# Optimization experiments

Hardware: AMD Instinct MI355X
Metric: run time of the kernel (lower is better)

The kernel has to match this reference:

```python
import jax, jax.numpy as jnp
import numpy as np

B, N = 1, 512
NODE_DIM, EDGE_DIM = 384, 128
H, SK, SV, PK, PV = 8, 16, 16, 4, 4
EPS = 1e-8
LN_EPS = 1e-5


def setup_inputs() -> dict:
    key = jax.random.key(0)
    ks = jax.random.split(key, 20)
    d, e = NODE_DIM, EDGE_DIM
    s = 0.02
    rn = lambda k, sh: jax.random.normal(k, sh, jnp.float32) * s
    # orthonormal per-residue rotations (valid rigid frames)
    R, _ = jnp.linalg.qr(jax.random.normal(ks[2], (B, N, 3, 3), jnp.float32))
    out_dim = H * (SV + EDGE_DIM + PV * 4)  # scalar + pairwise + points(3) + point norms(1)
    return dict(
        node_features=jax.random.normal(ks[0], (B, N, d), jnp.float32),
        edge_features=jax.random.normal(ks[1], (B, N, N, e), jnp.float32),
        rotations=R,
        translations=jax.random.normal(ks[3], (B, N, 3), jnp.float32),
        mask=jnp.ones((B, N), bool),
        Wq_s=rn(ks[4], (d, H * SK)), Wk_s=rn(ks[5], (d, H * SK)), Wv_s=rn(ks[6], (d, H * SV)),
        Wq_p=rn(ks[7], (d, H * PK * 3)), Wk_p=rn(ks[8], (d, H * PK * 3)), Wv_p=rn(ks[9], (d, H * PV * 3)),
        point_weights=jnp.full((H,), np.log(np.e - 1.0), jnp.float32),  # softplus -> 1
        Wb=rn(ks[10], (e, H)), bb=jnp.zeros((H,), jnp.float32),
        Wo=rn(ks[11], (out_dim, d)), bo=jnp.zeros((d,), jnp.float32),
        g1=jnp.ones((d,), jnp.float32), beta1=jnp.zeros((d,), jnp.float32),
        W1=rn(ks[12], (d, 2 * d)), b1=jnp.zeros((2 * d,), jnp.float32),
        W2=rn(ks[13], (2 * d, 2 * d)), b2=jnp.zeros((2 * d,), jnp.float32),
        W3=rn(ks[14], (2 * d, d)), b3=jnp.zeros((d,), jnp.float32),
        g2=jnp.ones((d,), jnp.float32), beta2=jnp.zeros((d,), jnp.float32),
    )


def _layer_norm(x, g, b):
    mu = x.mean(-1, keepdims=True)
    var = ((x - mu) ** 2).mean(-1, keepdims=True)
    return (x - mu) * jax.lax.rsqrt(var + LN_EPS) * g + b


def _forward(node_features, edge_features, rotations, translations, mask,
             Wq_s, Wk_s, Wv_s, Wq_p, Wk_p, Wv_p, point_weights, Wb, bb, Wo, bo,
             g1, beta1, W1, b1, W2, b2, W3, b3, g2, beta2):
    b, n, d = node_features.shape
    # num_attn_logits = 3 (scalar + point + pairwise)
    scal_scale = (3 * SK) ** -0.5
    point_scale = (3 * PK * 4.5) ** -0.5
    pair_scale = 3 ** -0.5

    qs = (node_features @ Wq_s).reshape(b, n, H, SK)
    kk = (node_features @ Wk_s).reshape(b, n, H, SK)
    vs = (node_features @ Wv_s).reshape(b, n, H, SV)

    def apply_rigid(p):  # p: (b,n,h,d,3); global = R^T applied per lucidrains einsum + t
        return jnp.einsum('bnhdc,bncr->bnhdr', p, rotations) + translations[:, :, None, None, :]

    qp = apply_rigid((node_features @ Wq_p).reshape(b, n, H, PK, 3))
    kp = apply_rigid((node_features @ Wk_p).reshape(b, n, H, PK, 3))
    vp = apply_rigid((node_features @ Wv_p).reshape(b, n, H, PV, 3))

    logits = jnp.einsum('bihk,bjhk->bhij', qs, kk) * scal_scale

    # point distance term: sum_{d,c} (q-k)^2 = |q|^2 + |k|^2 - 2 q.k (avoids (b,h,i,j,d,3) tensor)
    w = jax.nn.softplus(point_weights)  # (H,)
    q2 = jnp.einsum('bnhdc,bnhdc->bhn', qp, qp)
    k2 = jnp.einsum('bnhdc,bnhdc->bhn', kp, kp)
    cross = jnp.einsum('bihdc,bjhdc->bhij', qp, kp)
    dist = q2[..., :, None] + k2[..., None, :] - 2.0 * cross  # (b,h,i,j)
    logits = logits - 0.5 * point_scale * w[None, :, None, None] * dist

    pair_bias = (jnp.einsum('bije,eh->bhij', edge_features, Wb) + bb[None, :, None, None]) * pair_scale
    logits = logits + pair_bias

    pm = mask[:, None, :, None] & mask[:, None, None, :]  # (b,1,i,j)
    logits = jnp.where(pm, logits, -jnp.finfo(logits.dtype).max)
    attn = jax.nn.softmax(logits, axis=-1)  # (b,h,i,j)

    rs = jnp.einsum('bhij,bjhv->bihv', attn, vs).reshape(b, n, H * SV)
    rp = jnp.einsum('bhij,bije->bihe', attn, edge_features).reshape(b, n, H * EDGE_DIM)
    pts = jnp.einsum('bhij,bjhdc->bihdc', attn, vp)
    # invert rigid: subtract t, apply R (inverse of R^T application)
    local = jnp.einsum('bihdc,birc->bihdr', pts - translations[:, :, None, None, :], rotations)
    norms = jnp.sqrt((local ** 2).sum(-1) + EPS)  # (b,n,H,PV)

    cat = jnp.concatenate([rs, local.reshape(b, n, H * PV * 3), norms.reshape(b, n, H * PV), rp], axis=-1)
    ipa_out = cat @ Wo + bo

    x = _layer_norm(ipa_out, g1, beta1)  # dropout is identity at eval
    x = jax.nn.relu(x @ W1 + b1)
    x = jax.nn.relu(x @ W2 + b2)
    x = x @ W3 + b3
    return _layer_norm(x, g2, beta2)


def reference(node_features, edge_features, rotations, translations, mask,
              Wq_s, Wk_s, Wv_s, Wq_p, Wk_p, Wv_p, point_weights, Wb, bb, Wo, bo,
              g1, beta1, W1, b1, W2, b2, W3, b3, g2, beta2):
    return _forward(node_features, edge_features, rotations, translations, mask,
                    Wq_s, Wk_s, Wv_s, Wq_p, Wk_p, Wv_p, point_weights, Wb, bb, Wo, bo,
                    g1, beta1, W1, b1, W2, b2, W3, b3, g2, beta2)
```

## Files before the change

### kernel.cpp

```cpp
#include <hip/hip_runtime.h>
#include <cstddef>

#define NN 512
#define DD 384
#define EE 128
#define HH 8
#define JSPLIT 16

static constexpr float SCAL_SCALE  = 0.1443375673f;
static constexpr float POINT_SCALE = 0.1360827635f;
static constexpr float PAIR_SCALE  = 0.5773502692f;
static constexpr float LN_EPS = 1e-5f;
static constexpr float EPS    = 1e-8f;

typedef __bf16 bf16x8 __attribute__((ext_vector_type(8)));
typedef float  f32x4  __attribute__((ext_vector_type(4)));

__device__ __forceinline__ unsigned short bf16_bits(float v) {
    union { __bf16 b; unsigned short s; } c; c.b = (__bf16)v; return c.s;
}
__device__ __forceinline__ float bits2f(unsigned u) {
    union { unsigned u; float f; } c; c.u = u; return c.f;
}

__global__ __launch_bounds__(256) void prep_weights_kernel(
    const float* __restrict__ Wo, const float* __restrict__ W1,
    const float* __restrict__ W2, const float* __restrict__ W3,
    const float* __restrict__ Wq_s, const float* __restrict__ Wk_s,
    const float* __restrict__ Wv_s,
    const float* __restrict__ Wq_p, const float* __restrict__ Wk_p,
    const float* __restrict__ Wv_p, const float* __restrict__ nf,
    unsigned short* __restrict__ WoT, unsigned short* __restrict__ W1T,
    unsigned short* __restrict__ W2T, unsigned short* __restrict__ W3T,
    unsigned short* __restrict__ WprojT, unsigned short* __restrict__ nfb)
{
    const int b = blockIdx.x;
    if (b >= 1884) {
        const int idx = (b - 1884) * 1024 + threadIdx.x * 4;
        float4 v = *(const float4*)(nf + idx);
        unsigned lo = bf16_bits(v.x) | ((unsigned)bf16_bits(v.y) << 16);
        unsigned hi = bf16_bits(v.z) | ((unsigned)bf16_bits(v.w) << 16);
        uint2 pk; pk.x = lo; pk.y = hi;
        *(uint2*)(nfb + idx) = pk;
        return;
    }
    const float* W; unsigned short* out;
    int K, N, tile, rowoff = 0;
    if (b < 480)       { W = Wo;   out = WoT;    K = 1280; N = 384; tile = b; }
    else if (b < 768)  { W = W1;   out = W1T;    K = 384;  N = 768; tile = b - 480; }
    else if (b < 1344) { W = W2;   out = W2T;    K = 768;  N = 768; tile = b - 768; }
    else if (b < 1632) { W = W3;   out = W3T;    K = 768;  N = 384; tile = b - 1344; }
    else if (b < 1680) { W = Wq_s; out = WprojT; K = 384;  N = 128; tile = b - 1632; rowoff = 0; }
    else if (b < 1728) { W = Wk_s; out = WprojT; K = 384;  N = 128; tile = b - 1680; rowoff = 128; }
    else if (b < 1776) { W = Wv_s; out = WprojT; K = 384;  N = 128; tile = b - 1728; rowoff = 256; }
    else if (b < 1812) { W = Wq_p; out = WprojT; K = 384;  N = 96;  tile = b - 1776; rowoff = 384; }
    else if (b < 1848) { W = Wk_p; out = WprojT; K = 384;  N = 96;  tile = b - 1812; rowoff = 480; }
    else               { W = Wv_p; out = WprojT; K = 384;  N = 96;  tile = b - 1848; rowoff = 576; }

    const int ntn = N / 32;
    const int n0 = (tile % ntn) * 32, k0 = (tile / ntn) * 32;
    __shared__ float tb[32][33];
    const int tx = threadIdx.x & 31, ty = threadIdx.x >> 5;
    #pragma unroll
    for (int dy = 0; dy < 32; dy += 8)
        tb[ty + dy][tx] = W[(size_t)(k0 + ty + dy) * N + n0 + tx];
    __syncthreads();
    #pragma unroll
    for (int dy = 0; dy < 32; dy += 8)
        out[(size_t)(rowoff + n0 + ty + dy) * K + k0 + tx] = bf16_bits(tb[tx][ty + dy]);
}

template <int K, int NOUT, bool RELU, bool HASB, bool OUTBF>
__global__ __launch_bounds__(256) void gemm_bf16(
    const unsigned short* __restrict__ Xb, const unsigned short* __restrict__ Wt,
    const float* __restrict__ bias, void* __restrict__ Yv)
{
    const int t = threadIdx.x;
    const int w = t >> 6, lane = t & 63;
    const int r = lane & 15, q = lane >> 4;
    const int n0 = blockIdx.x * 16;
    const int m0 = blockIdx.y * 64 + w * 16;

    const unsigned short* xrow = Xb + (size_t)(m0 + r) * K + q * 8;
    const unsigned short* wrow = Wt + (size_t)(n0 + r) * K + q * 8;

    f32x4 acc = {0.f, 0.f, 0.f, 0.f};
    #pragma unroll 4
    for (int k0 = 0; k0 < K; k0 += 32) {
        union { uint4 u; bf16x8 v; } au, bu;
        au.u = *(const uint4*)(xrow + k0);
        bu.u = *(const uint4*)(wrow + k0);
        acc = __builtin_amdgcn_mfma_f32_16x16x32_bf16(au.v, bu.v, acc, 0, 0, 0);
    }
    const int n = n0 + r;
    const float bi = HASB ? bias[n] : 0.f;
    #pragma unroll
    for (int reg = 0; reg < 4; reg++) {
        const int m = m0 + q * 4 + reg;
        float v = acc[reg] + bi;
        if (RELU) v = fmaxf(v, 0.f);
        if (OUTBF) ((unsigned short*)Yv)[(size_t)m * NOUT + n] = bf16_bits(v);
        else       ((float*)Yv)[(size_t)m * NOUT + n] = v;
    }
}

__global__ __launch_bounds__(256) void ipa_post_kernel(
    const float* __restrict__ proj_out, const float* __restrict__ rot,
    const float* __restrict__ trans, const float* __restrict__ pw,
    const float* __restrict__ bb,
    unsigned short* __restrict__ Qp, unsigned short* __restrict__ Kp,
    unsigned short* __restrict__ svT)
{
    const int i = blockIdx.x;
    const int t = threadIdx.x;
    __shared__ float outs[672];
    __shared__ float ptg[288];
    __shared__ float q2s[8], k2s[8], pwh[8];

    for (int f = t; f < 672; f += 256) outs[f] = proj_out[(size_t)i * 672 + f];
    if (t < 8) pwh[t] = 0.5f * POINT_SCALE * log1pf(expf(pw[t]));
    __syncthreads();

    for (int f = t; f < 288; f += 256) {
        int which = f / 96, idx = f % 96;
        int hd = idx / 3, r = idx % 3;
        float acc = trans[(size_t)i * 3 + r];
        #pragma unroll
        for (int c = 0; c < 3; c++)
            acc += outs[384 + which * 96 + hd * 3 + c] * rot[(size_t)i * 9 + c * 3 + r];
        ptg[f] = acc;
    }
    __syncthreads();
    if (t < 16) {
        int which = t / 8, h = t % 8;
        float acc = 0.f;
        #pragma unroll
        for (int m = 0; m < 12; m++) {
            float v = ptg[which * 96 + h * 12 + m];
            acc += v * v;
        }
        (which ? k2s : q2s)[h] = acc;
    }
    __syncthreads();

    {
        const int h = t >> 5, d = t & 31;
        float qv, kv;
        if (d < 16)      { qv = outs[h * 16 + d] * SCAL_SCALE; kv = outs[128 + h * 16 + d]; }
        else if (d < 28) { qv = ptg[h * 12 + d - 16] * (2.f * pwh[h]); kv = ptg[96 + h * 12 + d - 16]; }
        else if (d == 28){ qv = -pwh[h] * q2s[h]; kv = 1.f; }
        else if (d == 29){ qv = 1.f; kv = -pwh[h] * k2s[h]; }
        else if (d == 30){ qv = 1.f; kv = bb[h] * PAIR_SCALE; }
        else             { qv = 0.f; kv = 0.f; }
        Qp[((size_t)i * 8 + h) * 32 + d] = bf16_bits(qv);
        Kp[((size_t)i * 8 + h) * 32 + d] = bf16_bits(kv);
    }
    if (t < 128) {
        int h = t >> 4, v = t & 15;
        svT[((size_t)h * 32 + v) * NN + i] = bf16_bits(outs[256 + h * 16 + v]);
    } else if (t < 224) {
        int idx = t - 128, h = idx / 12, m = idx % 12;
        svT[((size_t)h * 32 + 16 + m) * NN + i] = bf16_bits(ptg[192 + idx]);
    }
}

__global__ __launch_bounds__(256) void ipa_fused2(
    const float* __restrict__ edge,
    const unsigned short* __restrict__ Qp, const unsigned short* __restrict__ Kp,
    const unsigned short* __restrict__ svT, const float* __restrict__ Wb,
    float* __restrict__ Opart, float* __restrict__ Mpart, float* __restrict__ Lpart)
{
    const int js = blockIdx.x;
    const int it = blockIdx.y;
    const int i0 = it * 8;
    const int jbase = js * 32;
    const int t = threadIdx.x;
    const int w = t >> 6, lane = t & 63;
    const int r = lane & 15, q = lane >> 4;

    __shared__ unsigned short wbT[16 * 128];
    __shared__ unsigned short edA[64 * 128];
    __shared__ float Lqk[64 * 37];
    __shared__ float Lb[64 * 9];
    __shared__ unsigned short svj[8 * 8 * 32];
    __shared__ float mrow[64], lrow[64], arow[64];

    for (int idx = t; idx < 2048; idx += 256) {
        int h = idx >> 7, e = idx & 127;
        wbT[idx] = bf16_bits((h < 8) ? Wb[e * 8 + h] * PAIR_SCALE : 0.f);
    }
    if (t < 64) { mrow[t] = -1e30f; lrow[t] = 0.f; }
    __syncthreads();

    bf16x8 wbf[4];
    #pragma unroll
    for (int s = 0; s < 4; s++)
        wbf[s] = *(const bf16x8*)&wbT[r * 128 + s * 32 + q * 8];

    #pragma unroll
    for (int hh = 0; hh < 2; hh++) {
        const int h = w * 2 + hh;
        bf16x8 aq = *(const bf16x8*)&Qp[((size_t)(i0 + (r & 7)) * 8 + h) * 32 + q * 8];
        #pragma unroll
        for (int jt = 0; jt < 2; jt++) {
            bf16x8 bk = *(const bf16x8*)&Kp[((size_t)(jbase + jt * 16 + r) * 8 + h) * 32 + q * 8];
            f32x4 acc = {0.f, 0.f, 0.f, 0.f};
            acc = __builtin_amdgcn_mfma_f32_16x16x32_bf16(aq, bk, acc, 0, 0, 0);
            if (q < 2) {
                #pragma unroll
                for (int reg = 0; reg < 4; reg++)
                    Lqk[(h * 8 + q * 4 + reg) * 37 + jt * 16 + r] = acc[reg];
            }
        }
    }

    const int sj = t >> 5, sih = (t >> 4) & 1, sseg = t & 15;
    const int hsv = t / 28, csv = t % 28;
    float4 pf[8];
    uint4 svpf;
    {
        const int j0 = jbase;
        #pragma unroll
        for (int il = 0; il < 4; il++) {
            const float* src = edge + (((size_t)(i0 + sih * 4 + il) * NN) + (j0 + sj)) * EE + sseg * 8;
            pf[il * 2]     = *(const float4*)src;
            pf[il * 2 + 1] = *(const float4*)(src + 4);
        }
        if (t < 224) svpf = *(const uint4*)&svT[(size_t)(hsv * 32 + csv) * NN + j0];
    }

    const int ai = t >> 5, ah = (t >> 2) & 7, ap = t & 3;
    const int prow = ah * 8 + ai;
    float rp[32];
    float sva[8];
    #pragma unroll
    for (int z = 0; z < 32; z++) rp[z] = 0.f;
    #pragma unroll
    for (int s = 0; s < 8; s++) sva[s] = 0.f;

    for (int st = 0; st < 4; st++) {
        __syncthreads();
        #pragma unroll
        for (int il = 0; il < 4; il++) {
            const int row = sj * 8 + sih * 4 + il;
            union { bf16x8 v; uint4 u; } pk;
            pk.v[0] = (__bf16)pf[il*2].x;   pk.v[1] = (__bf16)pf[il*2].y;
            pk.v[2] = (__bf16)pf[il*2].z;   pk.v[3] = (__bf16)pf[il*2].w;
            pk.v[4] = (__bf16)pf[il*2+1].x; pk.v[5] = (__bf16)pf[il*2+1].y;
            pk.v[6] = (__bf16)pf[il*2+1].z; pk.v[7] = (__bf16)pf[il*2+1].w;
            *(uint4*)&edA[row * 128 + ((sseg ^ (row & 15)) * 8)] = pk.u;
        }
        if (t < 224) {
            svj[(hsv * 8 + 0) * 32 + csv] = (unsigned short)(svpf.x & 0xffff);
            svj[(hsv * 8 + 1) * 32 + csv] = (unsigned short)(svpf.x >> 16);
            svj[(hsv * 8 + 2) * 32 + csv] = (unsigned short)(svpf.y & 0xffff);
            svj[(hsv * 8 + 3) * 32 + csv] = (unsigned short)(svpf.y >> 16);
            svj[(hsv * 8 + 4) * 32 + csv] = (unsigned short)(svpf.z & 0xffff);
            svj[(hsv * 8 + 5) * 32 + csv] = (unsigned short)(svpf.z >> 16);
            svj[(hsv * 8 + 6) * 32 + csv] = (unsigned short)(svpf.w & 0xffff);
            svj[(hsv * 8 + 7) * 32 + csv] = (unsigned short)(svpf.w >> 16);
        }
        if (st < 3) {
            const int j0 = jbase + (st + 1) * 8;
            #pragma unroll
            for (int il = 0; il < 4; il++) {
                const float* src = edge + (((size_t)(i0 + sih * 4 + il) * NN) + (j0 + sj)) * EE + sseg * 8;
                pf[il * 2]     = *(const float4*)src;
                pf[il * 2 + 1] = *(const float4*)(src + 4);
            }
            if (t < 224) svpf = *(const uint4*)&svT[(size_t)(hsv * 32 + csv) * NN + j0];
        }
        __syncthreads();

        {
            f32x4 acc = {0.f, 0.f, 0.f, 0.f};
            #pragma unroll
            for (int s = 0; s < 4; s++) {
                bf16x8 a = *(const bf16x8*)&edA[(w * 16 + r) * 128 + (((s * 4 + q) ^ r) * 8)];
                acc = __builtin_amdgcn_mfma_f32_16x16x32_bf16(a, wbf[s], acc, 0, 0, 0);
            }
            if (r < 8) {
                #pragma unroll
                for (int reg = 0; reg < 4; reg++) {
                    const int m = q * 4 + reg;
                    Lb[(r * 8 + (m & 7)) * 9 + (w * 2 + (m >> 3))] = acc[reg];
                }
            }
        }
        __syncthreads();

        if (t < 64) {
            float lg[8];
            float mx = -1e30f;
            #pragma unroll
            for (int j = 0; j < 8; j++) {
                lg[j] = Lb[t * 9 + j] + Lqk[t * 37 + st * 8 + j];
                mx = fmaxf(mx, lg[j]);
            }
            const float mnew = fmaxf(mrow[t], mx);
            const float al = __expf(mrow[t] - mnew);
            float sum = 0.f;
            #pragma unroll
            for (int j = 0; j < 8; j++) {
                float p = __expf(lg[j] - mnew);
                Lb[t * 9 + j] = p;
                sum += p;
            }
            lrow[t] = lrow[t] * al + sum;
            mrow[t] = mnew;
            arow[t] = al;
        }
        __syncthreads();

        const float al = arow[prow];
        float pj[8];
        #pragma unroll
        for (int j = 0; j < 8; j++) pj[j] = Lb[prow * 9 + j];
        #pragma unroll
        for (int z = 0; z < 32; z++) rp[z] *= al;
        #pragma unroll
        for (int s = 0; s < 8; s++) sva[s] *= al;

        #pragma unroll
        for (int j = 0; j < 8; j++) {
            const int row = j * 8 + ai;
            const float p = pj[j];
            #pragma unroll
            for (int u = 0; u < 4; u++) {
                uint4 ev = *(const uint4*)&edA[row * 128 + (((ap * 4 + u) ^ (row & 15)) * 8)];
                rp[u*8+0] += p * bits2f(ev.x << 16);
                rp[u*8+1] += p * bits2f(ev.x & 0xffff0000u);
                rp[u*8+2] += p * bits2f(ev.y << 16);
                rp[u*8+3] += p * bits2f(ev.y & 0xffff0000u);
                rp[u*8+4] += p * bits2f(ev.z << 16);
                rp[u*8+5] += p * bits2f(ev.z & 0xffff0000u);
                rp[u*8+6] += p * bits2f(ev.w << 16);
                rp[u*8+7] += p * bits2f(ev.w & 0xffff0000u);
            }
            uint4 sv = *(const uint4*)&svj[(ah * 8 + j) * 32 + ap * 8];
            sva[0] += p * bits2f(sv.x << 16);
            sva[1] += p * bits2f(sv.x & 0xffff0000u);
            sva[2] += p * bits2f(sv.y << 16);
            sva[3] += p * bits2f(sv.y & 0xffff0000u);
            sva[4] += p * bits2f(sv.z << 16);
            sva[5] += p * bits2f(sv.z & 0xffff0000u);
            sva[6] += p * bits2f(sv.w << 16);
            sva[7] += p * bits2f(sv.w & 0xffff0000u);
        }
    }

    float* orow = Opart + (size_t)((js * 64 + it) * 8 + ai) * 1248;
    #pragma unroll
    for (int u = 0; u < 8; u++) {
        f32x4 vv = {rp[u*4+0], rp[u*4+1], rp[u*4+2], rp[u*4+3]};
        *(f32x4*)&orow[ah * 156 + 28 + ap * 32 + u * 4] = vv;
    }
    {
        f32x4 v0 = {sva[0], sva[1], sva[2], sva[3]};
        if (ap < 3) {
            f32x4 v1 = {sva[4], sva[5], sva[6], sva[7]};
            *(f32x4*)&orow[ah * 156 + ap * 8]     = v0;
            *(f32x4*)&orow[ah * 156 + ap * 8 + 4] = v1;
        } else {
            *(f32x4*)&orow[ah * 156 + 24] = v0;
        }
    }
    if (t < 64) {
        Mpart[(size_t)(js * 64 + it) * 64 + t] = mrow[t];
        Lpart[(size_t)(js * 64 + it) * 64 + t] = lrow[t];
    }
}

__global__ __launch_bounds__(256) void ipa_merge(
    const float* __restrict__ Opart, const float* __restrict__ Mpart,
    const float* __restrict__ Lpart, const float* __restrict__ rot,
    const float* __restrict__ trans, unsigned short* __restrict__ cat_bf)
{
    const int i = blockIdx.x;
    const int itile = i >> 3, il = i & 7;
    const int t = threadIdx.x;
    __shared__ float wn[8 * JSPLIT];
    __shared__ float pts_s[96];

    if (t < 8) {
        const int h = t;
        float ms[JSPLIT], ls[JSPLIT], M = -1e30f;
        #pragma unroll
        for (int s = 0; s < JSPLIT; s++) {
            ms[s] = Mpart[(size_t)(s * 64 + itile) * 64 + h * 8 + il];
            ls[s] = Lpart[(size_t)(s * 64 + itile) * 64 + h * 8 + il];
            M = fmaxf(M, ms[s]);
        }
        float denom = 0.f, e[JSPLIT];
        #pragma unroll
        for (int s = 0; s < JSPLIT; s++) { e[s] = __expf(ms[s] - M); denom += e[s] * ls[s]; }
        const float inv = 1.f / denom;
        #pragma unroll
        for (int s = 0; s < JSPLIT; s++) wn[h * JSPLIT + s] = e[s] * inv;
    }
    __syncthreads();

    for (int col = t; col < 1248; col += 256) {
        const int h = col / 156, c = col % 156;
        float acc = 0.f;
        #pragma unroll
        for (int s = 0; s < JSPLIT; s++)
            acc += wn[h * JSPLIT + s] *
                   Opart[((size_t)(s * 64 + itile) * 8 + il) * 1248 + col];
        if (c < 16)      cat_bf[(size_t)i * 1280 + h * 16 + c] = bf16_bits(acc);
        else if (c < 28) pts_s[h * 12 + (c - 16)] = acc;
        else             cat_bf[(size_t)i * 1280 + 256 + h * 128 + (c - 28)] = bf16_bits(acc);
    }
    __syncthreads();

    const float* tr = trans + (size_t)i * 3;
    const float* R  = rot + (size_t)i * 9;
    if (t < 96) {
        int hd = t / 3, rr = t % 3;
        float acc = 0.f;
        #pragma unroll
        for (int c = 0; c < 3; c++)
            acc += (pts_s[hd * 3 + c] - tr[c]) * R[rr * 3 + c];
        cat_bf[(size_t)i * 1280 + 128 + t] = bf16_bits(acc);
    } else if (t < 128) {
        int pv = t - 96;
        float s = EPS;
        #pragma unroll
        for (int rr = 0; rr < 3; rr++) {
            float v = 0.f;
            #pragma unroll
            for (int c = 0; c < 3; c++)
                v += (pts_s[pv * 3 + c] - tr[c]) * R[rr * 3 + c];
            s += v * v;
        }
        cat_bf[(size_t)i * 1280 + 224 + pv] = bf16_bits(sqrtf(s));
    }
}

template <bool OUTBF>
__global__ __launch_bounds__(256) void ln_kernel(
    const float* __restrict__ X, const float* __restrict__ g,
    const float* __restrict__ beta, void* __restrict__ Yv, int Dim)
{
    __shared__ float red[4];
    __shared__ float bc;
    const int i = blockIdx.x;
    const int t = threadIdx.x;
    const float* x = X + (size_t)i * Dim;

    float s = 0.f;
    for (int k = t; k < Dim; k += 256) s += x[k];
    #pragma unroll
    for (int off = 32; off; off >>= 1) s += __shfl_down(s, off, 64);
    if ((t & 63) == 0) red[t >> 6] = s;
    __syncthreads();
    if (t == 0) bc = red[0] + red[1] + red[2] + red[3];
    __syncthreads();
    const float mu = bc / Dim;

    float v = 0.f;
    for (int k = t; k < Dim; k += 256) { float d = x[k] - mu; v += d * d; }
    #pragma unroll
    for (int off = 32; off; off >>= 1) v += __shfl_down(v, off, 64);
    __syncthreads();
    if ((t & 63) == 0) red[t >> 6] = v;
    __syncthreads();
    if (t == 0) bc = red[0] + red[1] + red[2] + red[3];
    __syncthreads();
    const float rstd = rsqrtf(bc / Dim + LN_EPS);

    for (int k = t; k < Dim; k += 256) {
        float val = (x[k] - mu) * rstd * g[k] + beta[k];
        if (OUTBF) ((unsigned short*)Yv)[(size_t)i * Dim + k] = bf16_bits(val);
        else       ((float*)Yv)[(size_t)i * Dim + k] = val;
    }
}

extern "C" void kernel_launch(void* const* d_in, const int* in_sizes, int n_in,
                              void* d_out, int out_size, void* d_ws, size_t ws_size,
                              hipStream_t stream)
{
    const float* nf    = (const float*)d_in[0];
    const float* edge  = (const float*)d_in[1];
    const float* rot   = (const float*)d_in[2];
    const float* trans = (const float*)d_in[3];
    const float* Wq_s = (const float*)d_in[5];
    const float* Wk_s = (const float*)d_in[6];
    const float* Wv_s = (const float*)d_in[7];
    const float* Wq_p = (const float*)d_in[8];
    const float* Wk_p = (const float*)d_in[9];
    const float* Wv_p = (const float*)d_in[10];
    const float* pw   = (const float*)d_in[11];
    const float* Wb   = (const float*)d_in[12];
    const float* bb   = (const float*)d_in[13];
    const float* Wo   = (const float*)d_in[14];
    const float* bo   = (const float*)d_in[15];
    const float* g1   = (const float*)d_in[16];
    const float* be1  = (const float*)d_in[17];
    const float* W1   = (const float*)d_in[18];
    const float* b1   = (const float*)d_in[19];
    const float* W2   = (const float*)d_in[20];
    const float* b2   = (const float*)d_in[21];
    const float* W3   = (const float*)d_in[22];
    const float* b3   = (const float*)d_in[23];
    const float* g2   = (const float*)d_in[24];
    const float* be2  = (const float*)d_in[25];

    float* ws = (float*)d_ws;
    float* proj_out = ws;
    float* ipa   = proj_out + 344064;
    float* y     = ipa + 196608;
    float* Opart = y + 196608;
    float* Mpart = Opart + 10223616;
    float* Lpart = Mpart + 65536;
    unsigned short* cat_bf = (unsigned short*)(Lpart + 65536);
    unsigned short* x1b = cat_bf + 655360;
    unsigned short* h1b = x1b + 196608;
    unsigned short* h2b = h1b + 393216;
    unsigned short* Qp  = h2b + 393216;
    unsigned short* Kp  = Qp + 131072;
    unsigned short* svT = Kp + 131072;
    unsigned short* WoT = svT + 131072;
    unsigned short* W1T = WoT + 491520;
    unsigned short* W2T = W1T + 294912;
    unsigned short* W3T = W2T + 589824;
    unsigned short* WprojT = W3T + 294912;
    unsigned short* nfb = WprojT + 258048;

    prep_weights_kernel<<<2076, 256, 0, stream>>>(Wo, W1, W2, W3,
                                                  Wq_s, Wk_s, Wv_s, Wq_p, Wk_p, Wv_p, nf,
                                                  WoT, W1T, W2T, W3T, WprojT, nfb);

    gemm_bf16<384, 672, false, false, false><<<dim3(42, 8), 256, 0, stream>>>(nfb, WprojT, nullptr, proj_out);

    ipa_post_kernel<<<NN, 256, 0, stream>>>(proj_out, rot, trans, pw, bb, Qp, Kp, svT);

    ipa_fused2<<<dim3(JSPLIT, 64), 256, 0, stream>>>(edge, Qp, Kp, svT, Wb,
                                                     Opart, Mpart, Lpart);

    ipa_merge<<<NN, 256, 0, stream>>>(Opart, Mpart, Lpart, rot, trans, cat_bf);

    gemm_bf16<1280, 384, false, true, false><<<dim3(24, 8), 256, 0, stream>>>(cat_bf, WoT, bo, ipa);
    ln_kernel<true><<<NN, 256, 0, stream>>>(ipa, g1, be1, x1b, 384);

    gemm_bf16<384, 768, true, true, true><<<dim3(48, 8), 256, 0, stream>>>(x1b, W1T, b1, h1b);
    gemm_bf16<768, 768, true, true, true><<<dim3(48, 8), 256, 0, stream>>>(h1b, W2T, b2, h2b);
    gemm_bf16<768, 384, false, true, false><<<dim3(24, 8), 256, 0, stream>>>(h2b, W3T, b3, y);

    ln_kernel<false><<<NN, 256, 0, stream>>>(y, g2, be2, d_out, 384);
}
```

Measured before the change: 346.0 us.

## Compute pairwise attention-weighted edge sum with MFMA instead of scalar FMAs

```diff
diff --git a/kernel.cpp b/kernel.cpp
--- a/kernel.cpp
+++ b/kernel.cpp
@@ -183,19 +183,16 @@
     __shared__ float Lqk[64 * 37];
     __shared__ float Lb[64 * 9];
     __shared__ unsigned short svj[8 * 8 * 32];
+    __shared__ __align__(16) unsigned short P1[8 * 16 * 32];
     __shared__ float mrow[64], lrow[64], arow[64];
 
     for (int idx = t; idx < 2048; idx += 256) {
         int h = idx >> 7, e = idx & 127;
         wbT[idx] = bf16_bits((h < 8) ? Wb[e * 8 + h] * PAIR_SCALE : 0.f);
+        ((unsigned*)P1)[idx] = 0u;
     }
     if (t < 64) { mrow[t] = -1e30f; lrow[t] = 0.f; }
     __syncthreads();
-
-    bf16x8 wbf[4];
-    #pragma unroll
-    for (int s = 0; s < 4; s++)
-        wbf[s] = *(const bf16x8*)&wbT[r * 128 + s * 32 + q * 8];
 
     #pragma unroll
     for (int hh = 0; hh < 2; hh++) {
@@ -231,12 +228,16 @@
 
     const int ai = t >> 5, ah = (t >> 2) & 7, ap = t & 3;
     const int prow = ah * 8 + ai;
-    float rp[32];
     float sva[8];
     #pragma unroll
-    for (int z = 0; z < 32; z++) rp[z] = 0.f;
-    #pragma unroll
     for (int s = 0; s < 8; s++) sva[s] = 0.f;
+
+    f32x4 acc[2][8];
+    #pragma unroll
+    for (int ii = 0; ii < 2; ii++)
+        #pragma unroll
+        for (int eb = 0; eb < 8; eb++)
+            acc[ii][eb] = (f32x4){0.f, 0.f, 0.f, 0.f};
 
     for (int st = 0; st < 4; st++) {
         __syncthreads();
@@ -273,17 +274,18 @@
         __syncthreads();
 
         {
-            f32x4 acc = {0.f, 0.f, 0.f, 0.f};
+            f32x4 accb = {0.f, 0.f, 0.f, 0.f};
             #pragma unroll
             for (int s = 0; s < 4; s++) {
-                bf16x8 a = *(const bf16x8*)&edA[(w * 16 + r) * 128 + (((s * 4 + q) ^ r) * 8)];
-                acc = __builtin_amdgcn_mfma_f32_16x16x32_bf16(a, wbf[s], acc, 0, 0, 0);
+                bf16x8 a  = *(const bf16x8*)&edA[(w * 16 + r) * 128 + (((s * 4 + q) ^ r) * 8)];
+                bf16x8 wb = *(const bf16x8*)&wbT[r * 128 + s * 32 + q * 8];
+                accb = __builtin_amdgcn_mfma_f32_16x16x32_bf16(a, wb, accb, 0, 0, 0);
             }
             if (r < 8) {
                 #pragma unroll
                 for (int reg = 0; reg < 4; reg++) {
                     const int m = q * 4 + reg;
-                    Lb[(r * 8 + (m & 7)) * 9 + (w * 2 + (m >> 3))] = acc[reg];
+                    Lb[(r * 8 + (m & 7)) * 9 + (w * 2 + (m >> 3))] = accb[reg];
                 }
             }
         }
@@ -304,58 +306,76 @@
             for (int j = 0; j < 8; j++) {
                 float p = __expf(lg[j] - mnew);
                 Lb[t * 9 + j] = p;
+                lg[j] = p;
                 sum += p;
             }
             lrow[t] = lrow[t] * al + sum;
             mrow[t] = mnew;
             arow[t] = al;
+            unsigned* pw1 = (unsigned*)&P1[((((t & 7) << 4) | (t >> 3))) * 32];
+            pw1[0] = (unsigned)bf16_bits(lg[0]) | ((unsigned)bf16_bits(lg[1]) << 16);
+            pw1[1] = (unsigned)bf16_bits(lg[2]) | ((unsigned)bf16_bits(lg[3]) << 16);
+            pw1[2] = (unsigned)bf16_bits(lg[4]) | ((unsigned)bf16_bits(lg[5]) << 16);
+            pw1[3] = (unsigned)bf16_bits(lg[6]) | ((unsigned)bf16_bits(lg[7]) << 16);
         }
         __syncthreads();
 
-        const float al = arow[prow];
-        float pj[8];
-        #pragma unroll
-        for (int j = 0; j < 8; j++) pj[j] = Lb[prow * 9 + j];
-        #pragma unroll
-        for (int z = 0; z < 32; z++) rp[z] *= al;
-        #pragma unroll
-        for (int s = 0; s < 8; s++) sva[s] *= al;
-
-        #pragma unroll
-        for (int j = 0; j < 8; j++) {
-            const int row = j * 8 + ai;
-            const float p = pj[j];
-            #pragma unroll
-            for (int u = 0; u < 4; u++) {
-                uint4 ev = *(const uint4*)&edA[row * 128 + (((ap * 4 + u) ^ (row & 15)) * 8)];
-                rp[u*8+0] += p * bits2f(ev.x << 16);
-                rp[u*8+1] += p * bits2f(ev.x & 0xffff0000u);
-                rp[u*8+2] += p * bits2f(ev.y << 16);
-                rp[u*8+3] += p * bits2f(ev.y & 0xffff0000u);
-                rp[u*8+4] += p * bits2f(ev.z << 16);
-                rp[u*8+5] += p * bits2f(ev.z & 0xffff0000u);
-                rp[u*8+6] += p * bits2f(ev.w << 16);
-                rp[u*8+7] += p * bits2f(ev.w & 0xffff0000u);
-            }
-            uint4 sv = *(const uint4*)&svj[(ah * 8 + j) * 32 + ap * 8];
-            sva[0] += p * bits2f(sv.x << 16);
-            sva[1] += p * bits2f(sv.x & 0xffff0000u);
-            sva[2] += p * bits2f(sv.y << 16);
-            sva[3] += p * bits2f(sv.y & 0xffff0000u);
-            sva[4] += p * bits2f(sv.z << 16);
-            sva[5] += p * bits2f(sv.z & 0xffff0000u);
-            sva[6] += p * bits2f(sv.w << 16);
-            sva[7] += p * bits2f(sv.w & 0xffff0000u);
-        }
-    }
-
-    float* orow = Opart + (size_t)((js * 64 + it) * 8 + ai) * 1248;
-    #pragma unroll
-    for (int u = 0; u < 8; u++) {
-        f32x4 vv = {rp[u*4+0], rp[u*4+1], rp[u*4+2], rp[u*4+3]};
-        *(f32x4*)&orow[ah * 156 + 28 + ap * 32 + u * 4] = vv;
-    }
+        #pragma unroll
+        for (int ii = 0; ii < 2; ii++) {
+            const int il = w * 2 + ii;
+            const float alh = arow[((r & 7) << 3) + il];
+            union { uint4 u; bf16x8 v; } bP;
+            bP.u = *(const uint4*)&P1[((il << 4) + r) * 32 + q * 8];
+            #pragma unroll
+            for (int eb = 0; eb < 8; eb++) {
+                const int seg = eb * 2 + (r >> 3);
+                const int e7 = r & 7;
+                union { uint4 u; bf16x8 v; } af;
+                #define GA(m) ((unsigned)edA[((m)*8 + il) * 128 + (((seg) ^ (((m)*8 + il) & 15)) << 3) + e7])
+                af.u.x = GA(0) | (GA(1) << 16);
+                af.u.y = GA(2) | (GA(3) << 16);
+                af.u.z = GA(4) | (GA(5) << 16);
+                af.u.w = GA(6) | (GA(7) << 16);
+                #undef GA
+                f32x4 c = acc[ii][eb];
+                c[0] *= alh; c[1] *= alh; c[2] *= alh; c[3] *= alh;
+                acc[ii][eb] = __builtin_amdgcn_mfma_f32_16x16x32_bf16(af.v, bP.v, c, 0, 0, 0);
+            }
+        }
+
+        {
+            const float al = arow[prow];
+            #pragma unroll
+            for (int s = 0; s < 8; s++) sva[s] *= al;
+            #pragma unroll
+            for (int j = 0; j < 8; j++) {
+                const float p = Lb[prow * 9 + j];
+                uint4 sv = *(const uint4*)&svj[(ah * 8 + j) * 32 + ap * 8];
+                sva[0] += p * bits2f(sv.x << 16);
+                sva[1] += p * bits2f(sv.x & 0xffff0000u);
+                sva[2] += p * bits2f(sv.y << 16);
+                sva[3] += p * bits2f(sv.y & 0xffff0000u);
+                sva[4] += p * bits2f(sv.z << 16);
+                sva[5] += p * bits2f(sv.z & 0xffff0000u);
+                sva[6] += p * bits2f(sv.w << 16);
+                sva[7] += p * bits2f(sv.w & 0xffff0000u);
+            }
+        }
+    }
+
+    #pragma unroll
+    for (int ii = 0; ii < 2; ii++) {
+        const int il = w * 2 + ii;
+        float* orw = Opart + (size_t)((js * 64 + it) * 8 + il) * 1248;
+        if (r < 8) {
+            #pragma unroll
+            for (int eb = 0; eb < 8; eb++)
+                *(f32x4*)&orw[r * 156 + 28 + eb * 16 + q * 4] = acc[ii][eb];
+        }
+    }
+
     {
+        float* orow = Opart + (size_t)((js * 64 + it) * 8 + ai) * 1248;
         f32x4 v0 = {sva[0], sva[1], sva[2], sva[3]};
         if (ap < 3) {
             f32x4 v1 = {sva[4], sva[5], sva[6], sva[7]};
```

Result: faster. 335.3 us (-3.1%).

## Pre-transpose edges to bf16 and compute pair bias in a separate prep kernel

Applied to the files above, without the earlier changes.

```diff
diff --git a/kernel.cpp b/kernel.cpp
--- a/kernel.cpp
+++ b/kernel.cpp
@@ -70,6 +70,79 @@
         out[(size_t)(rowoff + n0 + ty + dy) * K + k0 + tx] = bf16_bits(tb[tx][ty + dy]);
 }
 
+__global__ __launch_bounds__(256) void edge_prep_kernel(
+    const float* __restrict__ edge, const float* __restrict__ Wb,
+    unsigned short* __restrict__ edgeT, float* __restrict__ biasG)
+{
+    const int bi = blockIdx.x;
+    const int i = bi >> 2, jt = bi & 3;
+    const int j0 = jt * 128;
+    const int t = threadIdx.x;
+    const int w = t >> 6, lane = t & 63, r = lane & 15, q = lane >> 4;
+
+    __shared__ float ldsT[32][33];
+    __shared__ unsigned short wbTl[16 * 128];
+
+    if (t < 128) {
+        float4 a = *(const float4*)&Wb[t * 8];
+        float4 b = *(const float4*)&Wb[t * 8 + 4];
+        wbTl[0 * 128 + t] = bf16_bits(a.x * PAIR_SCALE);
+        wbTl[1 * 128 + t] = bf16_bits(a.y * PAIR_SCALE);
+        wbTl[2 * 128 + t] = bf16_bits(a.z * PAIR_SCALE);
+        wbTl[3 * 128 + t] = bf16_bits(a.w * PAIR_SCALE);
+        wbTl[4 * 128 + t] = bf16_bits(b.x * PAIR_SCALE);
+        wbTl[5 * 128 + t] = bf16_bits(b.y * PAIR_SCALE);
+        wbTl[6 * 128 + t] = bf16_bits(b.z * PAIR_SCALE);
+        wbTl[7 * 128 + t] = bf16_bits(b.w * PAIR_SCALE);
+    } else {
+        const int z = t - 128;
+        #pragma unroll
+        for (int s = 0; s < 8; s++) wbTl[1024 + z * 8 + s] = 0;
+    }
+
+    const float* etile = edge + ((size_t)i * 512 + j0) * 128;
+
+    for (int sub = 0; sub < 16; sub++) {
+        const int jb = (sub >> 2) * 32, eb = (sub & 3) * 32;
+        __syncthreads();
+        {
+            const int jl = t >> 3, e4 = (t & 7) * 4;
+            *(float4*)&ldsT[jl][e4] = *(const float4*)&etile[(size_t)(jb + jl) * 128 + eb + e4];
+        }
+        __syncthreads();
+        if (t < 128) {
+            const int e = t >> 2, jseg = (t & 3) * 8;
+            union { uint4 u; unsigned short s[8]; } pk;
+            #pragma unroll
+            for (int s = 0; s < 8; s++) pk.s[s] = bf16_bits(ldsT[jseg + s][e]);
+            *(uint4*)&edgeT[((size_t)i * 128 + eb + e) * 512 + j0 + jb + jseg] = pk.u;
+        }
+    }
+    __syncthreads();
+
+    #pragma unroll
+    for (int rr = 0; rr < 2; rr++) {
+        const int rt = w * 2 + rr;
+        f32x4 acc = {0.f, 0.f, 0.f, 0.f};
+        #pragma unroll
+        for (int kk = 0; kk < 4; kk++) {
+            const float* src = &etile[(size_t)(rt * 16 + r) * 128 + kk * 32 + q * 8];
+            float4 f0 = *(const float4*)src;
+            float4 f1 = *(const float4*)(src + 4);
+            union { uint4 u; bf16x8 v; } aE;
+            aE.u.x = (unsigned)bf16_bits(f0.x) | ((unsigned)bf16_bits(f0.y) << 16);
+            aE.u.y = (unsigned)bf16_bits(f0.z) | ((unsigned)bf16_bits(f0.w) << 16);
+            aE.u.z = (unsigned)bf16_bits(f1.x) | ((unsigned)bf16_bits(f1.y) << 16);
+            aE.u.w = (unsigned)bf16_bits(f1.z) | ((unsigned)bf16_bits(f1.w) << 16);
+            union { uint4 u; bf16x8 v; } bW;
+            bW.u = *(const uint4*)&wbTl[r * 128 + kk * 32 + q * 8];
+            acc = __builtin_amdgcn_mfma_f32_16x16x32_bf16(aE.v, bW.v, acc, 0, 0, 0);
+        }
+        if (r < 8)
+            *(f32x4*)&biasG[((size_t)i * 8 + r) * 512 + j0 + rt * 16 + q * 4] = acc;
+    }
+}
+
 template <int K, int NOUT, bool RELU, bool HASB, bool OUTBF>
 __global__ __launch_bounds__(256) void gemm_bf16(
     const unsigned short* __restrict__ Xb, const unsigned short* __restrict__ Wt,
@@ -161,13 +234,17 @@
     } else if (t < 224) {
         int idx = t - 128, h = idx / 12, m = idx % 12;
         svT[((size_t)h * 32 + 16 + m) * NN + i] = bf16_bits(ptg[192 + idx]);
+    } else {
+        int idx = t - 224;
+        int h = idx >> 2, m = 28 + (idx & 3);
+        svT[((size_t)h * 32 + m) * NN + i] = 0;
     }
 }
 
 __global__ __launch_bounds__(256) void ipa_fused2(
-    const float* __restrict__ edge,
+    const unsigned short* __restrict__ edgeT, const float* __restrict__ biasG,
     const unsigned short* __restrict__ Qp, const unsigned short* __restrict__ Kp,
-    const unsigned short* __restrict__ svT, const float* __restrict__ Wb,
+    const unsigned short* __restrict__ svT,
     float* __restrict__ Opart, float* __restrict__ Mpart, float* __restrict__ Lpart)
 {
     const int js = blockIdx.x;
@@ -178,24 +255,15 @@
     const int w = t >> 6, lane = t & 63;
     const int r = lane & 15, q = lane >> 4;
 
-    __shared__ unsigned short wbT[16 * 128];
-    __shared__ unsigned short edA[64 * 128];
     __shared__ float Lqk[64 * 37];
-    __shared__ float Lb[64 * 9];
-    __shared__ unsigned short svj[8 * 8 * 32];
-    __shared__ float mrow[64], lrow[64], arow[64];
-
-    for (int idx = t; idx < 2048; idx += 256) {
-        int h = idx >> 7, e = idx & 127;
-        wbT[idx] = bf16_bits((h < 8) ? Wb[e * 8 + h] * PAIR_SCALE : 0.f);
-    }
-    if (t < 64) { mrow[t] = -1e30f; lrow[t] = 0.f; }
-    __syncthreads();
-
-    bf16x8 wbf[4];
-    #pragma unroll
-    for (int s = 0; s < 4; s++)
-        wbf[s] = *(const bf16x8*)&wbT[r * 128 + s * 32 + q * 8];
+    __shared__ __align__(16) unsigned short P1[8 * 16 * 32];
+    __shared__ __align__(16) unsigned short P2[8 * 16 * 32];
+
+    {
+        uint4 z = {0u, 0u, 0u, 0u};
+        uint4* p1 = (uint4*)P1; uint4* p2 = (uint4*)P2;
+        for (int k = t; k < 512; k += 256) { p1[k] = z; p2[k] = z; }
+    }
 
     #pragma unroll
     for (int hh = 0; hh < 2; hh++) {
@@ -213,161 +281,81 @@
             }
         }
     }
-
-    const int sj = t >> 5, sih = (t >> 4) & 1, sseg = t & 15;
-    const int hsv = t / 28, csv = t % 28;
-    float4 pf[8];
-    uint4 svpf;
-    {
-        const int j0 = jbase;
-        #pragma unroll
-        for (int il = 0; il < 4; il++) {
-            const float* src = edge + (((size_t)(i0 + sih * 4 + il) * NN) + (j0 + sj)) * EE + sseg * 8;
-            pf[il * 2]     = *(const float4*)src;
-            pf[il * 2 + 1] = *(const float4*)(src + 4);
-        }
-        if (t < 224) svpf = *(const uint4*)&svT[(size_t)(hsv * 32 + csv) * NN + j0];
-    }
-
-    const int ai = t >> 5, ah = (t >> 2) & 7, ap = t & 3;
-    const int prow = ah * 8 + ai;
-    float rp[32];
-    float sva[8];
-    #pragma unroll
-    for (int z = 0; z < 32; z++) rp[z] = 0.f;
-    #pragma unroll
-    for (int s = 0; s < 8; s++) sva[s] = 0.f;
-
-    for (int st = 0; st < 4; st++) {
-        __syncthreads();
-        #pragma unroll
-        for (int il = 0; il < 4; il++) {
-            const int row = sj * 8 + sih * 4 + il;
-            union { bf16x8 v; uint4 u; } pk;
-            pk.v[0] = (__bf16)pf[il*2].x;   pk.v[1] = (__bf16)pf[il*2].y;
-            pk.v[2] = (__bf16)pf[il*2].z;   pk.v[3] = (__bf16)pf[il*2].w;
-            pk.v[4] = (__bf16)pf[il*2+1].x; pk.v[5] = (__bf16)pf[il*2+1].y;
-            pk.v[6] = (__bf16)pf[il*2+1].z; pk.v[7] = (__bf16)pf[il*2+1].w;
-            *(uint4*)&edA[row * 128 + ((sseg ^ (row & 15)) * 8)] = pk.u;
-        }
-        if (t < 224) {
-            svj[(hsv * 8 + 0) * 32 + csv] = (unsigned short)(svpf.x & 0xffff);
-            svj[(hsv * 8 + 1) * 32 + csv] = (unsigned short)(svpf.x >> 16);
-            svj[(hsv * 8 + 2) * 32 + csv] = (unsigned short)(svpf.y & 0xffff);
-            svj[(hsv * 8 + 3) * 32 + csv] = (unsigned short)(svpf.y >> 16);
-            svj[(hsv * 8 + 4) * 32 + csv] = (unsigned short)(svpf.z & 0xffff);
-            svj[(hsv * 8 + 5) * 32 + csv] = (unsigned short)(svpf.z >> 16);
-            svj[(hsv * 8 + 6) * 32 + csv] = (unsigned short)(svpf.w & 0xffff);
-            svj[(hsv * 8 + 7) * 32 + csv] = (unsigned short)(svpf.w >> 16);
-        }
-        if (st < 3) {
-            const int j0 = jbase + (st + 1) * 8;
+    __syncthreads();
+
+    if (t < 64) {
+        const int h = t >> 3, i = t & 7;
+        const float* brow = biasG + ((size_t)(i0 + i) * 8 + h) * 512 + jbase;
+        float lg[32];
+        float mx = -1e30f;
+        #pragma unroll
+        for (int j = 0; j < 32; j++) {
+            lg[j] = Lqk[t * 37 + j] + brow[j];
+            mx = fmaxf(mx, lg[j]);
+        }
+        float sum = 0.f;
+        #pragma unroll
+        for (int j = 0; j < 32; j++) { lg[j] = __expf(lg[j] - mx); sum += lg[j]; }
+        Mpart[(size_t)(js * 64 + it) * 64 + t] = mx;
+        Lpart[(size_t)(js * 64 + it) * 64 + t] = sum;
+        unsigned pk[16];
+        #pragma unroll
+        for (int s = 0; s < 16; s++)
+            pk[s] = (unsigned)bf16_bits(lg[2 * s]) | ((unsigned)bf16_bits(lg[2 * s + 1]) << 16);
+        uint4* d1 = (uint4*)&P1[((size_t)i * 16 + h) * 32];
+        uint4* d2 = (uint4*)&P2[((size_t)h * 16 + i) * 32];
+        #pragma unroll
+        for (int s = 0; s < 4; s++) {
+            uint4 v; v.x = pk[4*s]; v.y = pk[4*s+1]; v.z = pk[4*s+2]; v.w = pk[4*s+3];
+            d1[s] = v; d2[s] = v;
+        }
+    }
+    __syncthreads();
+
+    #pragma unroll
+    for (int ii = 0; ii < 2; ii++) {
+        const int il = w * 2 + ii;
+        const unsigned short* eT = edgeT + ((size_t)(i0 + il) * 128) * 512 + jbase;
+        union { uint4 u; bf16x8 v; } bP;
+        bP.u = *(const uint4*)&P1[((size_t)il * 16 + r) * 32 + q * 8];
+        union { uint4 u; bf16x8 v; } aF[8];
+        #pragma unroll
+        for (int eb = 0; eb < 8; eb++)
+            aF[eb].u = *(const uint4*)&eT[(size_t)(eb * 16 + r) * 512 + q * 8];
+        f32x4 acc[8];
+        #pragma unroll
+        for (int eb = 0; eb < 8; eb++) {
+            f32x4 c = {0.f, 0.f, 0.f, 0.f};
+            acc[eb] = __builtin_amdgcn_mfma_f32_16x16x32_bf16(aF[eb].v, bP.v, c, 0, 0, 0);
+        }
+        float* orw = Opart + (size_t)((js * 64 + it) * 8 + il) * 1248;
+        if (r < 8) {
             #pragma unroll
-            for (int il = 0; il < 4; il++) {
-                const float* src = edge + (((size_t)(i0 + sih * 4 + il) * NN) + (j0 + sj)) * EE + sseg * 8;
-                pf[il * 2]     = *(const float4*)src;
-                pf[il * 2 + 1] = *(const float4*)(src + 4);
-            }
-            if (t < 224) svpf = *(const uint4*)&svT[(size_t)(hsv * 32 + csv) * NN + j0];
-        }
-        __syncthreads();
-
-        {
-            f32x4 acc = {0.f, 0.f, 0.f, 0.f};
-            #pragma unroll
-            for (int s = 0; s < 4; s++) {
-                bf16x8 a = *(const bf16x8*)&edA[(w * 16 + r) * 128 + (((s * 4 + q) ^ r) * 8)];
-                acc = __builtin_amdgcn_mfma_f32_16x16x32_bf16(a, wbf[s], acc, 0, 0, 0);
-            }
-            if (r < 8) {
+            for (int eb = 0; eb < 8; eb++)
+                *(f32x4*)&orw[r * 156 + 28 + eb * 16 + q * 4] = acc[eb];
+        }
+    }
+
+    #pragma unroll
+    for (int hh = 0; hh < 2; hh++) {
+        const int h = w * 2 + hh;
+        union { uint4 u; bf16x8 v; } aP;
+        aP.u = *(const uint4*)&P2[((size_t)h * 16 + r) * 32 + q * 8];
+        #pragma unroll
+        for (int ct = 0; ct < 2; ct++) {
+            union { uint4 u; bf16x8 v; } bS;
+            bS.u = *(const uint4*)&svT[((size_t)h * 32 + ct * 16 + r) * 512 + jbase + q * 8];
+            f32x4 c = {0.f, 0.f, 0.f, 0.f};
+            f32x4 acc = __builtin_amdgcn_mfma_f32_16x16x32_bf16(aP.v, bS.v, c, 0, 0, 0);
+            const int cc = ct * 16 + r;
+            if (q < 2 && cc < 28) {
                 #pragma unroll
                 for (int reg = 0; reg < 4; reg++) {
-                    const int m = q * 4 + reg;
-                    Lb[(r * 8 + (m & 7)) * 9 + (w * 2 + (m >> 3))] = acc[reg];
+                    const int i = q * 4 + reg;
+                    Opart[((size_t)((js * 64 + it) * 8 + i)) * 1248 + h * 156 + cc] = acc[reg];
                 }
             }
         }
-        __syncthreads();
-
-        if (t < 64) {
-            float lg[8];
-            float mx = -1e30f;
-            #pragma unroll
-            for (int j = 0; j < 8; j++) {
-                lg[j] = Lb[t * 9 + j] + Lqk[t * 37 + st * 8 + j];
-                mx = fmaxf(mx, lg[j]);
-            }
-            const float mnew = fmaxf(mrow[t], mx);
-            const float al = __expf(mrow[t] - mnew);
-            float sum = 0.f;
-            #pragma unroll
-            for (int j = 0; j < 8; j++) {
-                float p = __expf(lg[j] - mnew);
-                Lb[t * 9 + j] = p;
-                sum += p;
-            }
-            lrow[t] = lrow[t] * al + sum;
-            mrow[t] = mnew;
-            arow[t] = al;
-        }
-        __syncthreads();
-
-        const float al = arow[prow];
-        float pj[8];
-        #pragma unroll
-        for (int j = 0; j < 8; j++) pj[j] = Lb[prow * 9 + j];
-        #pragma unroll
-        for (int z = 0; z < 32; z++) rp[z] *= al;
-        #pragma unroll
-        for (int s = 0; s < 8; s++) sva[s] *= al;
-
-        #pragma unroll
-        for (int j = 0; j < 8; j++) {
-            const int row = j * 8 + ai;
-            const float p = pj[j];
-            #pragma unroll
-            for (int u = 0; u < 4; u++) {
-                uint4 ev = *(const uint4*)&edA[row * 128 + (((ap * 4 + u) ^ (row & 15)) * 8)];
-                rp[u*8+0] += p * bits2f(ev.x << 16);
-                rp[u*8+1] += p * bits2f(ev.x & 0xffff0000u);
-                rp[u*8+2] += p * bits2f(ev.y << 16);
-                rp[u*8+3] += p * bits2f(ev.y & 0xffff0000u);
-                rp[u*8+4] += p * bits2f(ev.z << 16);
-                rp[u*8+5] += p * bits2f(ev.z & 0xffff0000u);
-                rp[u*8+6] += p * bits2f(ev.w << 16);
-                rp[u*8+7] += p * bits2f(ev.w & 0xffff0000u);
-            }
-            uint4 sv = *(const uint4*)&svj[(ah * 8 + j) * 32 + ap * 8];
-            sva[0] += p * bits2f(sv.x << 16);
-            sva[1] += p * bits2f(sv.x & 0xffff0000u);
-            sva[2] += p * bits2f(sv.y << 16);
-            sva[3] += p * bits2f(sv.y & 0xffff0000u);
-            sva[4] += p * bits2f(sv.z << 16);
-            sva[5] += p * bits2f(sv.z & 0xffff0000u);
-            sva[6] += p * bits2f(sv.w << 16);
-            sva[7] += p * bits2f(sv.w & 0xffff0000u);
-        }
-    }
-
-    float* orow = Opart + (size_t)((js * 64 + it) * 8 + ai) * 1248;
-    #pragma unroll
-    for (int u = 0; u < 8; u++) {
-        f32x4 vv = {rp[u*4+0], rp[u*4+1], rp[u*4+2], rp[u*4+3]};
-        *(f32x4*)&orow[ah * 156 + 28 + ap * 32 + u * 4] = vv;
-    }
-    {
-        f32x4 v0 = {sva[0], sva[1], sva[2], sva[3]};
-        if (ap < 3) {
-            f32x4 v1 = {sva[4], sva[5], sva[6], sva[7]};
-            *(f32x4*)&orow[ah * 156 + ap * 8]     = v0;
-            *(f32x4*)&orow[ah * 156 + ap * 8 + 4] = v1;
-        } else {
-            *(f32x4*)&orow[ah * 156 + 24] = v0;
-        }
-    }
-    if (t < 64) {
-        Mpart[(size_t)(js * 64 + it) * 64 + t] = mrow[t];
-        Lpart[(size_t)(js * 64 + it) * 64 + t] = lrow[t];
     }
 }
 
@@ -526,6 +514,10 @@
     unsigned short* W3T = W2T + 589824;
     unsigned short* WprojT = W3T + 294912;
     unsigned short* nfb = WprojT + 258048;
+    unsigned short* edgeT = nfb + 196608;
+    float* biasG = (float*)(edgeT + 33554432);
+
+    edge_prep_kernel<<<2048, 256, 0, stream>>>(edge, Wb, edgeT, biasG);
 
     prep_weights_kernel<<<2076, 256, 0, stream>>>(Wo, W1, W2, W3,
                                                   Wq_s, Wk_s, Wv_s, Wq_p, Wk_p, Wv_p, nf,
@@ -535,7 +527,7 @@
 
     ipa_post_kernel<<<NN, 256, 0, stream>>>(proj_out, rot, trans, pw, bb, Qp, Kp, svT);
 
-    ipa_fused2<<<dim3(JSPLIT, 64), 256, 0, stream>>>(edge, Qp, Kp, svT, Wb,
+    ipa_fused2<<<dim3(JSPLIT, 64), 256, 0, stream>>>(edgeT, biasG, Qp, Kp, svT,
                                                      Opart, Mpart, Lpart);
 
     ipa_merge<<<NN, 256, 0, stream>>>(Opart, Mpart, Lpart, rot, trans, cat_bf);
```

Result: slower. 396.1 us (+14.5%).
